# Performance work log

Hardware: AMD Instinct MI355X
Metric: run time of the kernel (lower is better)

Reference implementation:

```python
import jax, jax.numpy as jnp
import numpy as np

QUERY_DIM = 1024
CONTEXT_DIM = 1024
HEADS = 8
DIM_HEAD = 64
INNER = HEADS * DIM_HEAD  # 512
SCALE = DIM_HEAD ** -0.5


def setup_inputs() -> dict:
    key = jax.random.key(0)
    ks = jax.random.split(key, 7)
    B, N, M = 2, 2048, 2048
    x = jax.random.normal(ks[0], (B, N, QUERY_DIM), dtype=jnp.float32)
    context = jax.random.normal(ks[1], (B, M, CONTEXT_DIM), dtype=jnp.float32)
    # nn.Linear weights (stored as [out, in] in torch; we use [in, out] here)
    Wq = jax.random.normal(ks[2], (QUERY_DIM, INNER), dtype=jnp.float32) * (QUERY_DIM ** -0.5)
    Wk = jax.random.normal(ks[3], (CONTEXT_DIM, INNER), dtype=jnp.float32) * (CONTEXT_DIM ** -0.5)
    Wv = jax.random.normal(ks[4], (CONTEXT_DIM, INNER), dtype=jnp.float32) * (CONTEXT_DIM ** -0.5)
    Wo = jax.random.normal(ks[5], (INNER, QUERY_DIM), dtype=jnp.float32) * (INNER ** -0.5)
    bo = jax.random.normal(ks[6], (QUERY_DIM,), dtype=jnp.float32) * 0.01
    return {"x": x, "context": context, "Wq": Wq, "Wk": Wk, "Wv": Wv, "Wo": Wo, "bo": bo}


def reference(x, context, Wq, Wk, Wv, Wo, bo):
    B, N, _ = x.shape
    M = context.shape[1]
    # projections (no bias, matching nn.Linear(bias=False))
    q = (x @ Wq).reshape(B, N, HEADS, DIM_HEAD)          # b i h d
    k = (context @ Wk).reshape(B, M, HEADS, DIM_HEAD)    # b j h d
    v = (context @ Wv).reshape(B, M, HEADS, DIM_HEAD)    # b j h d
    # scores in fp32 (ATTN_PRECISION=='fp32' path)
    sim = jnp.einsum('bihd,bjhd->bhij', q.astype(jnp.float32), k.astype(jnp.float32)) * SCALE
    attn = jax.nn.softmax(sim, axis=-1).astype(v.dtype)  # b h i j
    out = jnp.einsum('bhij,bjhd->bihd', attn, v).reshape(B, N, INNER)
    return out @ Wo + bo  # dropout p=0.0 is identity
```

## Files before the change

### kernel.cpp

```cpp
#include <hip/hip_runtime.h>
#include <math.h>

typedef __bf16 bf16_t;
typedef __bf16 bf16x8 __attribute__((ext_vector_type(8)));
typedef __bf16 bf16x4 __attribute__((ext_vector_type(4)));
typedef float  f32x4  __attribute__((ext_vector_type(4)));

#define MFMA16(a, b, c) __builtin_amdgcn_mfma_f32_16x16x32_bf16((a), (b), (c), 0, 0, 0)

#define INNER   512
#define DHEAD   64
#define QSCALE  0.18033688f

__device__ __forceinline__ void g2l(const bf16_t* g, bf16_t* l) {
  __builtin_amdgcn_global_load_lds(
      (const __attribute__((address_space(1))) unsigned int*)g,
      (__attribute__((address_space(3))) unsigned int*)l, 16, 0, 0);
}

__global__ __launch_bounds__(256) void pre_k(const float* __restrict__ x,
                                             const float* __restrict__ ctx,
                                             const float* __restrict__ Wq,
                                             const float* __restrict__ Wk,
                                             const float* __restrict__ Wv,
                                             const float* __restrict__ Wo,
                                             bf16_t* __restrict__ xb,
                                             bf16_t* __restrict__ cb,
                                             bf16_t* __restrict__ WqT,
                                             bf16_t* __restrict__ WkT,
                                             bf16_t* __restrict__ WvT,
                                             bf16_t* __restrict__ WoT) {
  __shared__ float tile[64][65];
  int bx = blockIdx.x;
  if (bx < 8192) {
    const float* in = (bx >= 4096) ? ctx : x;
    bf16_t* out     = (bx >= 4096) ? cb  : xb;
    int i = (bx & 4095) * 256 + threadIdx.x;
    float4 f = ((const float4*)in)[i];
    bf16x4 v = { (bf16_t)f.x, (bf16_t)f.y, (bf16_t)f.z, (bf16_t)f.w };
    ((bf16x4*)out)[i] = v;
    return;
  }
  int t = bx - 8192;
  int z = t >> 7, bid = t & 127;
  const float* W; bf16_t* WT; int K, N;
  if (z == 0)      { W = Wq; WT = WqT; K = 1024; N = 512; }
  else if (z == 1) { W = Wk; WT = WkT; K = 1024; N = 512; }
  else if (z == 2) { W = Wv; WT = WvT; K = 1024; N = 512; }
  else             { W = Wo; WT = WoT; K = 512;  N = 1024; }
  int tK = K >> 6;
  int kt = bid % tK, nt = bid / tK;
  int k0 = kt << 6, n0 = nt << 6;
  for (int idx = threadIdx.x; idx < 4096; idx += 256) {
    int r = idx >> 6, c = idx & 63;
    tile[r][c] = W[(size_t)(k0 + r) * N + n0 + c];
  }
  __syncthreads();
  for (int idx = threadIdx.x; idx < 4096; idx += 256) {
    int r = idx >> 6, c = idx & 63;
    WT[(size_t)(n0 + r) * K + k0 + c] = (bf16_t)tile[c][r];
  }
}

__device__ __forceinline__ void gemm128(const bf16_t* __restrict__ A,
                                        const bf16_t* __restrict__ Bt,
                                        int K, int N, int row0, int n0,
                                        int mode, float scale,
                                        bf16_t* __restrict__ Cb,
                                        float* __restrict__ Cf,
                                        const float* __restrict__ bias) {
  __shared__ bf16_t As[2 * 128 * 64];
  __shared__ bf16_t Bs[2 * 128 * 64];
  const int tid = threadIdx.x;
  const int w = tid >> 6, lane = tid & 63, quad = lane >> 4, l16 = lane & 15;

  const int sr8  = lane >> 3;
  const int slog = ((lane & 7) ^ sr8) << 3;
  const bf16_t* ga = A  + (size_t)(row0 + w * 32 + sr8) * K + slog;
  const bf16_t* gb = Bt + (size_t)(n0   + w * 32 + sr8) * K + slog;
  bf16_t* lA = As + w * 2048;
  bf16_t* lB = Bs + w * 2048;

  f32x4 acc[4][4];
#pragma unroll
  for (int i = 0; i < 4; ++i)
#pragma unroll
    for (int j = 0; j < 4; ++j) acc[i][j] = f32x4{0.f, 0.f, 0.f, 0.f};

  const int mrow = (w & 1) << 6, ncol = (w >> 1) << 6;
  const int KT = K >> 6;

#pragma unroll
  for (int p = 0; p < 4; ++p) {
    g2l(ga + (size_t)(p * 8) * K, lA + p * 512);
    g2l(gb + (size_t)(p * 8) * K, lB + p * 512);
  }

  for (int kc = 0; kc < KT; ++kc) {
    const int cur = (kc & 1) * 8192, nxt = ((kc + 1) & 1) * 8192;
    __syncthreads();
    if (kc + 1 < KT) {
      const int k0 = (kc + 1) * 64;
#pragma unroll
      for (int p = 0; p < 4; ++p) {
        g2l(ga + (size_t)(p * 8) * K + k0, lA + nxt + p * 512);
        g2l(gb + (size_t)(p * 8) * K + k0, lB + nxt + p * 512);
      }
    }
#pragma unroll
    for (int ks = 0; ks < 2; ++ks) {
      const int phys = ((ks * 4 + quad) ^ (l16 & 7)) << 3;
      bf16x8 af[4], bfr[4];
#pragma unroll
      for (int i = 0; i < 4; ++i)
        af[i] = *(const bf16x8*)&As[cur + (mrow + i * 16 + l16) * 64 + phys];
#pragma unroll
      for (int j = 0; j < 4; ++j)
        bfr[j] = *(const bf16x8*)&Bs[cur + (ncol + j * 16 + l16) * 64 + phys];
#pragma unroll
      for (int i = 0; i < 4; ++i)
#pragma unroll
        for (int j = 0; j < 4; ++j)
          acc[i][j] = MFMA16(af[i], bfr[j], acc[i][j]);
    }
  }

#pragma unroll
  for (int i = 0; i < 4; ++i) {
    int row = row0 + mrow + i * 16 + quad * 4;
#pragma unroll
    for (int j = 0; j < 4; ++j) {
      int col = n0 + ncol + j * 16 + l16;
      if (mode == 2) {
        int bb = row >> 11, key = row & 2047;
        int hh = col >> 6,  d   = col & 63;
        bf16x4 v = { (bf16_t)acc[i][j][0], (bf16_t)acc[i][j][1],
                     (bf16_t)acc[i][j][2], (bf16_t)acc[i][j][3] };
        *(bf16x4*)&Cb[((size_t)((bb * 8 + hh) * 64 + d)) * 2048 + key] = v;
      } else {
#pragma unroll
        for (int r = 0; r < 4; ++r) {
          if (mode == 1) Cf[(size_t)(row + r) * N + col] = acc[i][j][r] + bias[col];
          else           Cb[(size_t)(row + r) * N + col] = (bf16_t)(acc[i][j][r] * scale);
        }
      }
    }
  }
}

__global__ __launch_bounds__(256, 2) void gemm_qkv_k(const bf16_t* __restrict__ xb,
                                                     const bf16_t* __restrict__ cb,
                                                     const bf16_t* __restrict__ WqT,
                                                     const bf16_t* __restrict__ WkT,
                                                     const bf16_t* __restrict__ WvT,
                                                     bf16_t* __restrict__ Qb,
                                                     bf16_t* __restrict__ Kb,
                                                     bf16_t* __restrict__ Vt) {
  int z = blockIdx.z;
  const bf16_t* A  = (z == 0) ? xb  : cb;
  const bf16_t* Bt = (z == 0) ? WqT : (z == 1) ? WkT : WvT;
  bf16_t* C        = (z == 0) ? Qb  : (z == 1) ? Kb  : Vt;
  int mode         = (z == 2) ? 2 : 0;
  float scale      = (z == 0) ? QSCALE : 1.0f;
  gemm128(A, Bt, 1024, 512, blockIdx.y * 128, blockIdx.x * 128, mode, scale,
          C, nullptr, nullptr);
}

__global__ __launch_bounds__(256, 2) void gemm_out_k(const bf16_t* __restrict__ AO,
                                                     const bf16_t* __restrict__ WoT,
                                                     const float* __restrict__ bo,
                                                     float* __restrict__ out) {
  gemm128(AO, WoT, 512, 1024, blockIdx.y * 128, blockIdx.x * 128, 1, 1.0f,
          nullptr, out, bo);
}

__global__ __launch_bounds__(256, 2) void attn_k(const bf16_t* __restrict__ Qb,
                                                 const bf16_t* __restrict__ Kb,
                                                 const bf16_t* __restrict__ Vt,
                                                 bf16_t* __restrict__ AO) {
  const int tid = threadIdx.x;
  const int w = tid >> 6, lane = tid & 63, quad = lane >> 4, l16 = lane & 15;
  const int qt = blockIdx.x;
  const int bh = blockIdx.y;
  const int b = bh >> 3, h = bh & 7;

  __shared__ bf16_t Ks[2 * 128 * 64];
  __shared__ bf16_t Vs[64 * 128];
  __shared__ bf16_t Ps[64 * 136];

  const int qrow = b * 2048 + qt * 64 + w * 16 + l16;
  const bf16_t* qptr = Qb + (size_t)qrow * INNER + h * DHEAD;
  bf16x8 bq[2];
  bq[0] = *(const bf16x8*)(qptr + quad * 8);
  bq[1] = *(const bf16x8*)(qptr + 32 + quad * 8);

  f32x4 o[4];
#pragma unroll
  for (int dt = 0; dt < 4; ++dt) o[dt] = f32x4{0.f, 0.f, 0.f, 0.f};
  float m_s = -__builtin_inff(), l_s = 0.f;

  const bf16_t* kbase  = Kb + ((size_t)b * 2048) * INNER + h * DHEAD;
  const bf16_t* vtbase = Vt + ((size_t)bh * 64) * 2048;

  const int krow = lane >> 3;
  const int kcol = ((lane & 7) ^ (lane >> 3)) << 3;
  const int vrow = lane >> 4;

#pragma unroll
  for (int p = 0; p < 4; ++p)
    g2l(kbase + (size_t)(w * 32 + p * 8 + krow) * INNER + kcol,
        &Ks[w * 2048 + p * 512]);

  for (int kt = 0; kt < 16; ++kt) {
    const int cur = (kt & 1) * 8192, nxt = ((kt + 1) & 1) * 8192;
    __syncthreads();
    if (kt < 16 - 1) {
#pragma unroll
      for (int p = 0; p < 4; ++p)
        g2l(kbase + (size_t)((kt + 1) * 128 + w * 32 + p * 8 + krow) * INNER + kcol,
            &Ks[nxt + w * 2048 + p * 512]);
    }
#pragma unroll
    for (int p = 0; p < 4; ++p) {
      int vlog = ((lane & 15) ^ ((p * 4 + vrow) & 15)) << 3;
      g2l(vtbase + (size_t)(w * 16 + p * 4 + vrow) * 2048 + kt * 128 + vlog,
          &Vs[w * 2048 + p * 512]);
    }

    f32x4 s[8];
#pragma unroll
    for (int jt = 0; jt < 8; ++jt) s[jt] = f32x4{0.f, 0.f, 0.f, 0.f};
#pragma unroll
    for (int jt = 0; jt < 8; ++jt) {
#pragma unroll
      for (int ks = 0; ks < 2; ++ks) {
        int phys = ((ks * 4 + quad) ^ (l16 & 7)) << 3;
        bf16x8 ak = *(const bf16x8*)&Ks[cur + (jt * 16 + l16) * 64 + phys];
        s[jt] = MFMA16(ak, bq[ks], s[jt]);
      }
    }

    float mx = -__builtin_inff();
#pragma unroll
    for (int jt = 0; jt < 8; ++jt) {
      float a = fmaxf(fmaxf(s[jt][0], s[jt][1]), fmaxf(s[jt][2], s[jt][3]));
      mx = fmaxf(mx, a);
    }
    mx = fmaxf(mx, __shfl_xor(mx, 16, 64));
    mx = fmaxf(mx, __shfl_xor(mx, 32, 64));
    float mnew = fmaxf(m_s, mx);
    float alpha = __builtin_amdgcn_exp2f(m_s - mnew);
    float rs = 0.f;
#pragma unroll
    for (int jt = 0; jt < 8; ++jt) {
#pragma unroll
      for (int r = 0; r < 4; ++r) {
        float p = __builtin_amdgcn_exp2f(s[jt][r] - mnew);
        s[jt][r] = p;
        rs += p;
      }
    }
    rs += __shfl_xor(rs, 16, 64);
    rs += __shfl_xor(rs, 32, 64);
    l_s = l_s * alpha + rs;
    m_s = mnew;
#pragma unroll
    for (int dt = 0; dt < 4; ++dt) o[dt] *= alpha;

#pragma unroll
    for (int jt = 0; jt < 8; ++jt) {
      bf16x4 pk = { (bf16_t)s[jt][0], (bf16_t)s[jt][1],
                    (bf16_t)s[jt][2], (bf16_t)s[jt][3] };
      *(bf16x4*)&Ps[(w * 16 + l16) * 136 + jt * 16 + quad * 4] = pk;
    }

    __syncthreads();

#pragma unroll
    for (int kc = 0; kc < 4; ++kc) {
      bf16x8 bp = *(const bf16x8*)&Ps[(w * 16 + l16) * 136 + kc * 32 + quad * 8];
#pragma unroll
      for (int dt = 0; dt < 4; ++dt) {
        int phys = ((kc * 4 + quad) ^ l16) << 3;
        bf16x8 av = *(const bf16x8*)&Vs[(dt * 16 + l16) * 128 + phys];
        o[dt] = MFMA16(av, bp, o[dt]);
      }
    }
  }

  float inv = 1.0f / l_s;
#pragma unroll
  for (int dt = 0; dt < 4; ++dt) {
    bf16x4 ov = { (bf16_t)(o[dt][0] * inv), (bf16_t)(o[dt][1] * inv),
                  (bf16_t)(o[dt][2] * inv), (bf16_t)(o[dt][3] * inv) };
    *(bf16x4*)&Ps[(w * 16 + l16) * 136 + dt * 16 + quad * 4] = ov;
  }
  __syncthreads();
  {
    int sr = tid >> 2, sc = (tid & 3) << 4;
    int4 r0 = *(const int4*)&Ps[sr * 136 + sc];
    int4 r1 = *(const int4*)&Ps[sr * 136 + sc + 8];
    bf16_t* aout = AO + ((size_t)(b * 2048 + qt * 64 + sr)) * INNER + h * DHEAD + sc;
    *(int4*)aout       = r0;
    *(int4*)(aout + 8) = r1;
  }
}

extern "C" void kernel_launch(void* const* d_in, const int* in_sizes, int n_in,
                              void* d_out, int out_size, void* d_ws, size_t ws_size,
                              hipStream_t stream) {
  const float* x   = (const float*)d_in[0];
  const float* ctx = (const float*)d_in[1];
  const float* Wq  = (const float*)d_in[2];
  const float* Wk  = (const float*)d_in[3];
  const float* Wv  = (const float*)d_in[4];
  const float* Wo  = (const float*)d_in[5];
  const float* bo  = (const float*)d_in[6];
  float* out = (float*)d_out;

  char* ws = (char*)d_ws;
  const size_t MB = 1048576;
  bf16_t* xb  = (bf16_t*)(ws + 0 * MB);
  bf16_t* cb  = (bf16_t*)(ws + 8 * MB);
  bf16_t* WqT = (bf16_t*)(ws + 16 * MB);
  bf16_t* WkT = (bf16_t*)(ws + 17 * MB);
  bf16_t* WvT = (bf16_t*)(ws + 18 * MB);
  bf16_t* WoT = (bf16_t*)(ws + 19 * MB);
  bf16_t* Qb  = (bf16_t*)(ws + 20 * MB);
  bf16_t* Kb  = (bf16_t*)(ws + 24 * MB);
  bf16_t* Vt  = (bf16_t*)(ws + 28 * MB);
  bf16_t* AO  = (bf16_t*)(ws + 32 * MB);

  pre_k<<<8704, 256, 0, stream>>>(x, ctx, Wq, Wk, Wv, Wo, xb, cb, WqT, WkT, WvT, WoT);
  gemm_qkv_k<<<dim3(4, 32, 3), 256, 0, stream>>>(xb, cb, WqT, WkT, WvT, Qb, Kb, Vt);
  attn_k<<<dim3(32, 16), 256, 0, stream>>>(Qb, Kb, Vt, AO);
  gemm_out_k<<<dim3(8, 32), 256, 0, stream>>>(AO, WoT, bo, out);
}
```

Before: 165.5 us.

## Split attention over key dimension with a log-sum-exp merge kernel

The attention kernel now splits the 2048 keys into two halves via blockIdx.z, doubling the grid from 512 to 1024 blocks. Each half writes a partial normalized output plus a log-sum-exp weight, and a new merge kernel combines them into AO. Key tiles shrink to 64, K and V are both double-buffered, and the P tile becomes per-wave with no barrier before PV, so LDS use drops and occupancy rises to 4 blocks per CU. The cost is an extra kernel launch plus the partial-output traffic to global memory.

```diff
diff --git a/kernel.cpp b/kernel.cpp
--- a/kernel.cpp
+++ b/kernel.cpp
@@ -174,22 +174,24 @@
           nullptr, out, bo);
 }
 
-__global__ __launch_bounds__(256, 2) void attn_k(const bf16_t* __restrict__ Qb,
+__global__ __launch_bounds__(256, 4) void attn_k(const bf16_t* __restrict__ Qb,
                                                  const bf16_t* __restrict__ Kb,
                                                  const bf16_t* __restrict__ Vt,
-                                                 bf16_t* __restrict__ AO) {
+                                                 bf16_t* __restrict__ Op,
+                                                 float* __restrict__ Wgt) {
   const int tid = threadIdx.x;
   const int w = tid >> 6, lane = tid & 63, quad = lane >> 4, l16 = lane & 15;
   const int qt = blockIdx.x;
   const int bh = blockIdx.y;
+  const int z  = blockIdx.z;
   const int b = bh >> 3, h = bh & 7;
 
-  __shared__ bf16_t Ks[2 * 128 * 64];
-  __shared__ bf16_t Vs[64 * 128];
-  __shared__ bf16_t Ps[64 * 136];
-
-  const int qrow = b * 2048 + qt * 64 + w * 16 + l16;
-  const bf16_t* qptr = Qb + (size_t)qrow * INNER + h * DHEAD;
+  __shared__ bf16_t Ks[2][64 * 64];
+  __shared__ bf16_t Vs[2][64 * 64];
+  __shared__ bf16_t Ps[64 * 64];
+
+  const int qloc = qt * 64 + w * 16 + l16;
+  const bf16_t* qptr = Qb + (size_t)(b * 2048 + qloc) * INNER + h * DHEAD;
   bf16x8 bq[2];
   bq[0] = *(const bf16x8*)(qptr + quad * 8);
   bq[1] = *(const bf16x8*)(qptr + 32 + quad * 8);
@@ -199,50 +201,48 @@
   for (int dt = 0; dt < 4; ++dt) o[dt] = f32x4{0.f, 0.f, 0.f, 0.f};
   float m_s = -__builtin_inff(), l_s = 0.f;
 
-  const bf16_t* kbase  = Kb + ((size_t)b * 2048) * INNER + h * DHEAD;
-  const bf16_t* vtbase = Vt + ((size_t)bh * 64) * 2048;
-
-  const int krow = lane >> 3;
-  const int kcol = ((lane & 7) ^ (lane >> 3)) << 3;
-  const int vrow = lane >> 4;
-
-#pragma unroll
-  for (int p = 0; p < 4; ++p)
-    g2l(kbase + (size_t)(w * 32 + p * 8 + krow) * INNER + kcol,
-        &Ks[w * 2048 + p * 512]);
+  const bf16_t* kbase  = Kb + ((size_t)(b * 2048 + z * 1024)) * INNER + h * DHEAD;
+  const bf16_t* vtbase = Vt + ((size_t)bh * 64) * 2048 + z * 1024;
+
+  const int srow = lane >> 3;
+  const int slog = ((lane & 7) ^ srow) << 3;
+
+#pragma unroll
+  for (int p = 0; p < 2; ++p) {
+    int r = p * 32 + w * 8 + srow;
+    g2l(kbase + (size_t)r * INNER + slog, &Ks[0][(p * 32 + w * 8) * 64]);
+    g2l(vtbase + (size_t)r * 2048 + slog, &Vs[0][(p * 32 + w * 8) * 64]);
+  }
 
   for (int kt = 0; kt < 16; ++kt) {
-    const int cur = (kt & 1) * 8192, nxt = ((kt + 1) & 1) * 8192;
+    const int cur = kt & 1, nxt = (kt + 1) & 1;
     __syncthreads();
-    if (kt < 16 - 1) {
-#pragma unroll
-      for (int p = 0; p < 4; ++p)
-        g2l(kbase + (size_t)((kt + 1) * 128 + w * 32 + p * 8 + krow) * INNER + kcol,
-            &Ks[nxt + w * 2048 + p * 512]);
-    }
-#pragma unroll
-    for (int p = 0; p < 4; ++p) {
-      int vlog = ((lane & 15) ^ ((p * 4 + vrow) & 15)) << 3;
-      g2l(vtbase + (size_t)(w * 16 + p * 4 + vrow) * 2048 + kt * 128 + vlog,
-          &Vs[w * 2048 + p * 512]);
-    }
-
-    f32x4 s[8];
-#pragma unroll
-    for (int jt = 0; jt < 8; ++jt) s[jt] = f32x4{0.f, 0.f, 0.f, 0.f};
-#pragma unroll
-    for (int jt = 0; jt < 8; ++jt) {
+    if (kt + 1 < 16) {
+      const int k0 = (kt + 1) * 64;
+#pragma unroll
+      for (int p = 0; p < 2; ++p) {
+        int r = p * 32 + w * 8 + srow;
+        g2l(kbase + (size_t)(k0 + r) * INNER + slog, &Ks[nxt][(p * 32 + w * 8) * 64]);
+        g2l(vtbase + (size_t)r * 2048 + k0 + slog,   &Vs[nxt][(p * 32 + w * 8) * 64]);
+      }
+    }
+
+    f32x4 s[4];
+#pragma unroll
+    for (int jt = 0; jt < 4; ++jt) s[jt] = f32x4{0.f, 0.f, 0.f, 0.f};
+#pragma unroll
+    for (int jt = 0; jt < 4; ++jt) {
 #pragma unroll
       for (int ks = 0; ks < 2; ++ks) {
         int phys = ((ks * 4 + quad) ^ (l16 & 7)) << 3;
-        bf16x8 ak = *(const bf16x8*)&Ks[cur + (jt * 16 + l16) * 64 + phys];
+        bf16x8 ak = *(const bf16x8*)&Ks[cur][(jt * 16 + l16) * 64 + phys];
         s[jt] = MFMA16(ak, bq[ks], s[jt]);
       }
     }
 
     float mx = -__builtin_inff();
 #pragma unroll
-    for (int jt = 0; jt < 8; ++jt) {
+    for (int jt = 0; jt < 4; ++jt) {
       float a = fmaxf(fmaxf(s[jt][0], s[jt][1]), fmaxf(s[jt][2], s[jt][3]));
       mx = fmaxf(mx, a);
     }
@@ -252,7 +252,7 @@
     float alpha = __builtin_amdgcn_exp2f(m_s - mnew);
     float rs = 0.f;
 #pragma unroll
-    for (int jt = 0; jt < 8; ++jt) {
+    for (int jt = 0; jt < 4; ++jt) {
 #pragma unroll
       for (int r = 0; r < 4; ++r) {
         float p = __builtin_amdgcn_exp2f(s[jt][r] - mnew);
@@ -268,42 +268,57 @@
     for (int dt = 0; dt < 4; ++dt) o[dt] *= alpha;
 
 #pragma unroll
-    for (int jt = 0; jt < 8; ++jt) {
+    for (int jt = 0; jt < 4; ++jt) {
       bf16x4 pk = { (bf16_t)s[jt][0], (bf16_t)s[jt][1],
                     (bf16_t)s[jt][2], (bf16_t)s[jt][3] };
-      *(bf16x4*)&Ps[(w * 16 + l16) * 136 + jt * 16 + quad * 4] = pk;
-    }
-
-    __syncthreads();
-
-#pragma unroll
-    for (int kc = 0; kc < 4; ++kc) {
-      bf16x8 bp = *(const bf16x8*)&Ps[(w * 16 + l16) * 136 + kc * 32 + quad * 8];
+      int pc = (jt * 2 + (quad >> 1)) ^ (l16 & 7);
+      *(bf16x4*)&Ps[(w * 16 + l16) * 64 + pc * 8 + (quad & 1) * 4] = pk;
+    }
+
+#pragma unroll
+    for (int kc = 0; kc < 2; ++kc) {
+      int phys = ((kc * 4 + quad) ^ (l16 & 7)) << 3;
+      bf16x8 bp = *(const bf16x8*)&Ps[(w * 16 + l16) * 64 + phys];
 #pragma unroll
       for (int dt = 0; dt < 4; ++dt) {
-        int phys = ((kc * 4 + quad) ^ l16) << 3;
-        bf16x8 av = *(const bf16x8*)&Vs[(dt * 16 + l16) * 128 + phys];
+        bf16x8 av = *(const bf16x8*)&Vs[cur][(dt * 16 + l16) * 64 + phys];
         o[dt] = MFMA16(av, bp, o[dt]);
       }
     }
   }
 
   float inv = 1.0f / l_s;
+  size_t obase = ((size_t)(z * 16 + bh) * 2048 + qloc) * 64;
 #pragma unroll
   for (int dt = 0; dt < 4; ++dt) {
     bf16x4 ov = { (bf16_t)(o[dt][0] * inv), (bf16_t)(o[dt][1] * inv),
                   (bf16_t)(o[dt][2] * inv), (bf16_t)(o[dt][3] * inv) };
-    *(bf16x4*)&Ps[(w * 16 + l16) * 136 + dt * 16 + quad * 4] = ov;
-  }
-  __syncthreads();
-  {
-    int sr = tid >> 2, sc = (tid & 3) << 4;
-    int4 r0 = *(const int4*)&Ps[sr * 136 + sc];
-    int4 r1 = *(const int4*)&Ps[sr * 136 + sc + 8];
-    bf16_t* aout = AO + ((size_t)(b * 2048 + qt * 64 + sr)) * INNER + h * DHEAD + sc;
-    *(int4*)aout       = r0;
-    *(int4*)(aout + 8) = r1;
-  }
+    *(bf16x4*)&Op[obase + dt * 16 + quad * 4] = ov;
+  }
+  if (quad == 0)
+    Wgt[(size_t)(z * 16 + bh) * 2048 + qloc] = m_s + __builtin_amdgcn_logf(l_s);
+}
+
+__global__ __launch_bounds__(256) void merge_k(const bf16_t* __restrict__ Op,
+                                               const float* __restrict__ Wgt,
+                                               bf16_t* __restrict__ AO) {
+  int t = blockIdx.x * 256 + threadIdx.x;
+  int dg = t & 7, q = (t >> 3) & 2047, bh = t >> 14;
+  size_t r0 = (size_t)bh * 2048 + q;
+  bf16x8 o0 = *(const bf16x8*)&Op[r0 * 64 + dg * 8];
+  bf16x8 o1 = *(const bf16x8*)&Op[(size_t)2097152 + r0 * 64 + dg * 8];
+  float w0 = Wgt[r0], w1 = Wgt[32768 + r0];
+  float wm = fmaxf(w0, w1);
+  float a0 = __builtin_amdgcn_exp2f(w0 - wm);
+  float a1 = __builtin_amdgcn_exp2f(w1 - wm);
+  float inv = 1.0f / (a0 + a1);
+  a0 *= inv; a1 *= inv;
+  bf16x8 res;
+#pragma unroll
+  for (int i = 0; i < 8; ++i)
+    res[i] = (bf16_t)(a0 * (float)o0[i] + a1 * (float)o1[i]);
+  int b = bh >> 3, h = bh & 7;
+  *(bf16x8*)&AO[((size_t)(b * 2048 + q)) * INNER + h * DHEAD + dg * 8] = res;
 }
 
 extern "C" void kernel_launch(void* const* d_in, const int* in_sizes, int n_in,
@@ -330,9 +345,12 @@
   bf16_t* Kb  = (bf16_t*)(ws + 24 * MB);
   bf16_t* Vt  = (bf16_t*)(ws + 28 * MB);
   bf16_t* AO  = (bf16_t*)(ws + 32 * MB);
+  bf16_t* Op  = (bf16_t*)(ws + 36 * MB);
+  float*  Wgt = (float*)(ws + 44 * MB);
 
   pre_k<<<8704, 256, 0, stream>>>(x, ctx, Wq, Wk, Wv, Wo, xb, cb, WqT, WkT, WvT, WoT);
   gemm_qkv_k<<<dim3(4, 32, 3), 256, 0, stream>>>(xb, cb, WqT, WkT, WvT, Qb, Kb, Vt);
-  attn_k<<<dim3(32, 16), 256, 0, stream>>>(Qb, Kb, Vt, AO);
+  attn_k<<<dim3(32, 16, 2), 256, 0, stream>>>(Qb, Kb, Vt, Op, Wgt);
+  merge_k<<<1024, 256, 0, stream>>>(Op, Wgt, AO);
   gemm_out_k<<<dim3(8, 32), 256, 0, stream>>>(AO, WoT, bo, out);
 }
```

Result: slower. 169.1 us (+2.2%).

## Double-buffer V tiles, prefetch with K, and drop per-tile P barrier

Applied to the files above, without the earlier changes.

V tiles get their own double buffer and are prefetched one tile ahead alongside K, so the P·V product no longer waits on a V load issued in the same iteration. The padded P scratch becomes an XOR-swizzled 128-wide layout, and the __syncthreads between writing and reading P is removed because each wave only touches its own rows. The epilogue reuses Ps with a different 64-wide swizzled stride. Waves whose output rows overlap other waves' P rows can then race if a wave is still in its last P·V step. LDS use rises to about 80KB per block.

```diff
diff --git a/kernel.cpp b/kernel.cpp
--- a/kernel.cpp
+++ b/kernel.cpp
@@ -184,12 +184,12 @@
   const int bh = blockIdx.y;
   const int b = bh >> 3, h = bh & 7;
 
-  __shared__ bf16_t Ks[2 * 128 * 64];
-  __shared__ bf16_t Vs[64 * 128];
-  __shared__ bf16_t Ps[64 * 136];
-
-  const int qrow = b * 2048 + qt * 64 + w * 16 + l16;
-  const bf16_t* qptr = Qb + (size_t)qrow * INNER + h * DHEAD;
+  __shared__ bf16_t Ks[2][128 * 64];
+  __shared__ bf16_t Vs[2][64 * 128];
+  __shared__ bf16_t Ps[64 * 128];
+
+  const int qloc = qt * 64 + w * 16 + l16;
+  const bf16_t* qptr = Qb + (size_t)(b * 2048 + qloc) * INNER + h * DHEAD;
   bf16x8 bq[2];
   bq[0] = *(const bf16x8*)(qptr + quad * 8);
   bq[1] = *(const bf16x8*)(qptr + 32 + quad * 8);
@@ -203,28 +203,31 @@
   const bf16_t* vtbase = Vt + ((size_t)bh * 64) * 2048;
 
   const int krow = lane >> 3;
-  const int kcol = ((lane & 7) ^ (lane >> 3)) << 3;
+  const int kcol = ((lane & 7) ^ krow) << 3;
   const int vrow = lane >> 4;
 
 #pragma unroll
-  for (int p = 0; p < 4; ++p)
+  for (int p = 0; p < 4; ++p) {
     g2l(kbase + (size_t)(w * 32 + p * 8 + krow) * INNER + kcol,
-        &Ks[w * 2048 + p * 512]);
+        &Ks[0][(w * 32 + p * 8) * 64]);
+    int vlog = ((lane & 15) ^ ((p * 4 + vrow) & 15)) << 3;
+    g2l(vtbase + (size_t)(w * 16 + p * 4 + vrow) * 2048 + vlog,
+        &Vs[0][(w * 16 + p * 4) * 128]);
+  }
 
   for (int kt = 0; kt < 16; ++kt) {
-    const int cur = (kt & 1) * 8192, nxt = ((kt + 1) & 1) * 8192;
+    const int cur = kt & 1, nxt = (kt + 1) & 1;
     __syncthreads();
-    if (kt < 16 - 1) {
-#pragma unroll
-      for (int p = 0; p < 4; ++p)
-        g2l(kbase + (size_t)((kt + 1) * 128 + w * 32 + p * 8 + krow) * INNER + kcol,
-            &Ks[nxt + w * 2048 + p * 512]);
-    }
-#pragma unroll
-    for (int p = 0; p < 4; ++p) {
-      int vlog = ((lane & 15) ^ ((p * 4 + vrow) & 15)) << 3;
-      g2l(vtbase + (size_t)(w * 16 + p * 4 + vrow) * 2048 + kt * 128 + vlog,
-          &Vs[w * 2048 + p * 512]);
+    if (kt + 1 < 16) {
+      const int k0 = (kt + 1) * 128;
+#pragma unroll
+      for (int p = 0; p < 4; ++p) {
+        g2l(kbase + (size_t)(k0 + w * 32 + p * 8 + krow) * INNER + kcol,
+            &Ks[nxt][(w * 32 + p * 8) * 64]);
+        int vlog = ((lane & 15) ^ ((p * 4 + vrow) & 15)) << 3;
+        g2l(vtbase + (size_t)(w * 16 + p * 4 + vrow) * 2048 + k0 + vlog,
+            &Vs[nxt][(w * 16 + p * 4) * 128]);
+      }
     }
 
     f32x4 s[8];
@@ -235,7 +238,7 @@
 #pragma unroll
       for (int ks = 0; ks < 2; ++ks) {
         int phys = ((ks * 4 + quad) ^ (l16 & 7)) << 3;
-        bf16x8 ak = *(const bf16x8*)&Ks[cur + (jt * 16 + l16) * 64 + phys];
+        bf16x8 ak = *(const bf16x8*)&Ks[cur][(jt * 16 + l16) * 64 + phys];
         s[jt] = MFMA16(ak, bq[ks], s[jt]);
       }
     }
@@ -271,18 +274,17 @@
     for (int jt = 0; jt < 8; ++jt) {
       bf16x4 pk = { (bf16_t)s[jt][0], (bf16_t)s[jt][1],
                     (bf16_t)s[jt][2], (bf16_t)s[jt][3] };
-      *(bf16x4*)&Ps[(w * 16 + l16) * 136 + jt * 16 + quad * 4] = pk;
-    }
-
-    __syncthreads();
+      int pc = (jt * 2 + (quad >> 1)) ^ l16;
+      *(bf16x4*)&Ps[(w * 16 + l16) * 128 + pc * 8 + (quad & 1) * 4] = pk;
+    }
 
 #pragma unroll
     for (int kc = 0; kc < 4; ++kc) {
-      bf16x8 bp = *(const bf16x8*)&Ps[(w * 16 + l16) * 136 + kc * 32 + quad * 8];
+      int phys = ((kc * 4 + quad) ^ l16) << 3;
+      bf16x8 bp = *(const bf16x8*)&Ps[(w * 16 + l16) * 128 + phys];
 #pragma unroll
       for (int dt = 0; dt < 4; ++dt) {
-        int phys = ((kc * 4 + quad) ^ l16) << 3;
-        bf16x8 av = *(const bf16x8*)&Vs[(dt * 16 + l16) * 128 + phys];
+        bf16x8 av = *(const bf16x8*)&Vs[cur][(dt * 16 + l16) * 128 + phys];
         o[dt] = MFMA16(av, bp, o[dt]);
       }
     }
@@ -293,14 +295,17 @@
   for (int dt = 0; dt < 4; ++dt) {
     bf16x4 ov = { (bf16_t)(o[dt][0] * inv), (bf16_t)(o[dt][1] * inv),
                   (bf16_t)(o[dt][2] * inv), (bf16_t)(o[dt][3] * inv) };
-    *(bf16x4*)&Ps[(w * 16 + l16) * 136 + dt * 16 + quad * 4] = ov;
+    int pc = (dt * 2 + (quad >> 1)) ^ (l16 & 7);
+    *(bf16x4*)&Ps[(w * 16 + l16) * 64 + pc * 8 + (quad & 1) * 4] = ov;
   }
   __syncthreads();
   {
-    int sr = tid >> 2, sc = (tid & 3) << 4;
-    int4 r0 = *(const int4*)&Ps[sr * 136 + sc];
-    int4 r1 = *(const int4*)&Ps[sr * 136 + sc + 8];
-    bf16_t* aout = AO + ((size_t)(b * 2048 + qt * 64 + sr)) * INNER + h * DHEAD + sc;
+    int sr = tid >> 2, c2 = (tid & 3) * 2;
+    int p0 = (c2 ^ (sr & 7)) << 3, p1 = ((c2 + 1) ^ (sr & 7)) << 3;
+    int4 r0 = *(const int4*)&Ps[sr * 64 + p0];
+    int4 r1 = *(const int4*)&Ps[sr * 64 + p1];
+    bf16_t* aout = AO + ((size_t)(b * 2048 + qt * 64 + sr)) * INNER + h * DHEAD
+                      + (tid & 3) * 16;
     *(int4*)aout       = r0;
     *(int4*)(aout + 8) = r1;
   }
```

Measured after the change: 169.5 us. +2.4%, slower.
